# Kernel tuning notes

Hardware: AMD Instinct MI355X
Metric: run time of the kernel (lower is better)

The kernel has to match this reference:

```python
import jax, jax.numpy as jnp
import numpy as np

B, S, D, V = 512, 4096, 128, 6
SPARSITY = 0.1
PAD_IDX = 5


def setup_inputs() -> dict:
    key = jax.random.key(0)
    ks = jax.random.split(key, 16)
    n = lambda k, shape: (jax.random.normal(k, shape, jnp.float32) * 0.02)
    emb = n(ks[0], (V, D)).at[PAD_IDX].set(0.0)  # padding_idx=5 row zeroed
    # importance_network: D -> D/2 -> D/4 -> 1
    W1 = n(ks[1], (D, D // 2)); b1 = jnp.zeros((D // 2,), jnp.float32)
    W2 = n(ks[2], (D // 2, D // 4)); b2 = jnp.zeros((D // 4,), jnp.float32)
    W3 = n(ks[3], (D // 4, 1)); b3 = jnp.zeros((1,), jnp.float32)
    # attention_approximator: D -> D/2 -> D (dropout = identity in eval)
    A1 = n(ks[4], (D, D // 2)); a1 = jnp.zeros((D // 2,), jnp.float32)
    A2 = n(ks[5], (D // 2, D)); a2 = jnp.zeros((D,), jnp.float32)
    # classifier: D -> D/2 -> 1 -> sigmoid
    C1 = n(ks[6], (D, D // 2)); c1 = jnp.zeros((D // 2,), jnp.float32)
    C2 = n(ks[7], (D // 2, 1)); c2 = jnp.zeros((1,), jnp.float32)
    x = jax.random.randint(ks[8], (B, S), 0, V, dtype=jnp.int64 if jax.config.jax_enable_x64 else jnp.int32)
    return dict(x=x, emb=emb, W1=W1, b1=b1, W2=W2, b2=b2, W3=W3, b3=b3,
                A1=A1, a1=a1, A2=A2, a2=a2, C1=C1, c1=c1, C2=C2, c2=c2)


def reference(x, emb, W1, b1, W2, b2, W3, b3, A1, a1, A2, a2, C1, c1, C2, c2):
    batch, seq = x.shape
    k = max(1, int(seq * SPARSITY))  # 409
    e = emb[x]  # [B,S,D] embedding lookup
    # importance MLP + sigmoid -> learned scores [B,S]
    h = jax.nn.relu(e @ W1 + b1)
    h = jax.nn.relu(h @ W2 + b2)
    final_scores = jax.nn.sigmoid((h @ W3 + b3)[..., 0])  # [B,S]
    # topk select + gather embeddings (irregular access)
    top_vals, top_idx = jax.lax.top_k(final_scores, k)  # [B,k]
    sel = jnp.take_along_axis(e, top_idx[..., None], axis=1)  # [B,k,D]
    # attention approximator MLP
    attended = jax.nn.relu(sel @ A1 + a1) @ A2 + a2  # [B,k,D]
    pooled = attended.mean(axis=1)  # [B,D]
    # classifier
    pred = jax.nn.sigmoid((jax.nn.relu(pooled @ C1 + c1) @ C2 + c2))[..., 0]  # [B]
    return pred, top_idx, final_scores
```

## Files before the change

### kernel.cpp

```cpp
#include <hip/hip_runtime.h>
#include <hip/hip_bf16.h>
#include <math.h>

#define BB 512
#define SS 4096
#define DD 128
#define VV 6
#define KK 409



__global__ __launch_bounds__(256) void precompute_kernel(
    const float* __restrict__ emb,
    const float* __restrict__ W1, const float* __restrict__ b1,
    const float* __restrict__ W2, const float* __restrict__ b2,
    const float* __restrict__ W3, const float* __restrict__ b3,
    const float* __restrict__ A1, const float* __restrict__ a1,
    const float* __restrict__ A2, const float* __restrict__ a2,
    float* __restrict__ ws)
{
    __shared__ float sW1[DD * 64];
    __shared__ float sA1[DD * 64];
    __shared__ float sW2[64 * 32];
    __shared__ float sA2[64 * DD];
    __shared__ float sE[VV * DD];
    __shared__ float sW3[32];
    __shared__ float sb1[64], sb2[32], sa1[64], sa2[DD];
    __shared__ float sh1[VV * 64], sg[VV * 64], sh2[VV * 32];
    __shared__ float sb3;

    const int tid = threadIdx.x;

    {
        const float* srcs[9] = { W1, A1, W2, A2, emb, b1, b2, a1, a2 };
        float*       dsts[9] = { sW1, sA1, sW2, sA2, sE, sb1, sb2, sa1, sa2 };
        const int    ns[9]   = { 8192, 8192, 2048, 8192, VV*DD, 64, 32, 64, DD };
        for (int a = 0; a < 9; ++a) {
            const float4* s4 = (const float4*)srcs[a];
            float4* d4 = (float4*)dsts[a];
            const int n4 = ns[a] >> 2;
            for (int i = tid; i < n4; i += 256) d4[i] = s4[i];
        }
        if (tid < 32) sW3[tid] = W3[tid];
        if (tid == 0) sb3 = b3[0];
    }
    __syncthreads();

    for (int u = tid; u < 768; u += 256) {
        const int isH = (u < 384) ? 1 : 0;
        const int v = isH ? u : (u - 384);
        const int t = v >> 6, o = v & 63;
        const float* wcol = isH ? sW1 : sA1;
        float acc = isH ? sb1[o] : sa1[o];
        const float* ev = &sE[t * DD];
        #pragma unroll 8
        for (int d = 0; d < DD; ++d) acc += ev[d] * wcol[d * 64 + o];
        acc = fmaxf(acc, 0.f);
        if (isH) sh1[v] = acc; else sg[v] = acc;
    }
    __syncthreads();

    for (int u = tid; u < VV * 32; u += 256) {
        const int t = u >> 5, o = u & 31;
        float acc = sb2[o];
        #pragma unroll 8
        for (int j = 0; j < 64; ++j) acc += sh1[t * 64 + j] * sW2[j * 32 + o];
        sh2[u] = fmaxf(acc, 0.f);
    }
    __syncthreads();

    for (int u = tid; u < 6 + VV * DD; u += 256) {
        if (u < 6) {
            float s = sb3;
            #pragma unroll
            for (int j = 0; j < 32; ++j) s += sh2[u * 32 + j] * sW3[j];
            ws[u] = 1.f / (1.f + expf(-s));
        } else {
            const int v = u - 6;
            const int t = v >> 7, o = v & 127;
            float acc = sa2[o];
            #pragma unroll 8
            for (int j = 0; j < 64; ++j) acc += sg[t * 64 + j] * sA2[j * DD + o];
            ws[16 + v] = acc;
        }
    }
}

__global__ __launch_bounds__(512) void row_kernel(
    const int* __restrict__ x,
    const float* __restrict__ ws,
    const float* __restrict__ C1, const float* __restrict__ c1,
    const float* __restrict__ C2, const float* __restrict__ c2,
    float* __restrict__ pred, float* __restrict__ topk, float* __restrict__ fsc)
{
    __shared__ float sc[VV];
    __shared__ float att_s[VV * DD];
    __shared__ int   waveTot[8 * VV];
    __shared__ float pooled[DD];
    __shared__ float hcls[64];

    const int tid  = threadIdx.x;
    const int b    = blockIdx.x;
    const int lane = tid & 63;
    const int w    = tid >> 6;

    const int base = b * SS + tid * 8;
    const int4* xp = (const int4*)(x + base);
    int4 xv0 = xp[0], xv1 = xp[1];

    if (tid < VV) sc[tid] = ws[tid];
    for (int i = tid; i < VV * DD; i += 512) att_s[i] = ws[16 + i];
    __syncthreads();

    int vals[8];
    vals[0]=xv0.x; vals[1]=xv0.y; vals[2]=xv0.z; vals[3]=xv0.w;
    vals[4]=xv1.x; vals[5]=xv1.y; vals[6]=xv1.z; vals[7]=xv1.w;

    {
        float4* op = (float4*)(fsc + base);
        float4 o0, o1;
        o0.x = sc[vals[0]]; o0.y = sc[vals[1]]; o0.z = sc[vals[2]]; o0.w = sc[vals[3]];
        o1.x = sc[vals[4]]; o1.y = sc[vals[5]]; o1.z = sc[vals[6]]; o1.w = sc[vals[7]];
        op[0] = o0; op[1] = o1;
    }

    int lc[VV];
    #pragma unroll
    for (int t = 0; t < VV; ++t) {
        int c = 0;
        #pragma unroll
        for (int i = 0; i < 8; ++i) c += (vals[i] == t) ? 1 : 0;
        lc[t] = c;
    }

    int excl[VV];
    #pragma unroll
    for (int t = 0; t < VV; ++t) {
        int v = lc[t];
        #pragma unroll
        for (int off = 1; off < 64; off <<= 1) {
            int u = __shfl_up(v, off, 64);
            if (lane >= off) v += u;
        }
        excl[t] = v - lc[t];
        if (lane == 63) waveTot[w * VV + t] = v;
    }
    __syncthreads();

    int rowTot[VV], woff[VV];
    #pragma unroll
    for (int t = 0; t < VV; ++t) {
        int tot = 0, wo = 0;
        #pragma unroll
        for (int j = 0; j < 8; ++j) {
            int c = waveTot[j * VV + t];
            tot += c;
            if (j < 1) {}
            wo += (j < w) ? c : 0;
        }
        rowTot[t] = tot;
        woff[t] = wo;
    }

    float s_reg[VV];
    #pragma unroll
    for (int t = 0; t < VV; ++t) s_reg[t] = sc[t];
    int pri[VV];
    #pragma unroll
    for (int t = 0; t < VV; ++t) {
        int p = 0;
        #pragma unroll
        for (int u = 0; u < VV; ++u)
            p += ((s_reg[u] > s_reg[t]) || ((s_reg[u] == s_reg[t]) && (u < t))) ? 1 : 0;
        pri[t] = p;
    }
    int start[VV], m[VV];
    #pragma unroll
    for (int t = 0; t < VV; ++t) {
        int cb = 0;
        #pragma unroll
        for (int u = 0; u < VV; ++u)
            cb += (pri[u] < pri[t]) ? rowTot[u] : 0;
        int mm = KK - cb;
        mm = (mm < 0) ? 0 : mm;
        mm = (mm > rowTot[t]) ? rowTot[t] : mm;
        m[t] = mm;
        start[t] = cb + woff[t] + excl[t];
    }

    #pragma unroll
    for (int t = 0; t < VV; ++t) {
        int pos = start[t];
        #pragma unroll
        for (int i = 0; i < 8; ++i) {
            if (vals[i] == t) {
                if (pos < KK) topk[b * KK + pos] = (float)(tid * 8 + i);
                pos++;
            }
        }
    }

    if (tid < DD) {
        float acc = 0.f;
        #pragma unroll
        for (int t = 0; t < VV; ++t) acc += (float)m[t] * att_s[t * DD + tid];
        pooled[tid] = acc * (1.0f / (float)KK);
    }
    __syncthreads();
    if (tid < 64) {
        float acc = c1[tid];
        #pragma unroll 8
        for (int d = 0; d < DD; ++d) acc += pooled[d] * C1[d * 64 + tid];
        hcls[tid] = fmaxf(acc, 0.f);
    }
    __syncthreads();
    if (tid == 0) {
        float s = c2[0];
        #pragma unroll 8
        for (int j = 0; j < 64; ++j) s += hcls[j] * C2[j];
        pred[b] = 1.f / (1.f + expf(-s));
    }
}

extern "C" void kernel_launch(void* const* d_in, const int* in_sizes, int n_in,
                              void* d_out, int out_size, void* d_ws, size_t ws_size,
                              hipStream_t stream)
{
    (void)in_sizes; (void)n_in; (void)out_size; (void)ws_size;
    const int*   x   = (const int*)d_in[0];
    const float* emb = (const float*)d_in[1];
    const float* W1  = (const float*)d_in[2];
    const float* b1  = (const float*)d_in[3];
    const float* W2  = (const float*)d_in[4];
    const float* b2  = (const float*)d_in[5];
    const float* W3  = (const float*)d_in[6];
    const float* b3  = (const float*)d_in[7];
    const float* A1  = (const float*)d_in[8];
    const float* a1  = (const float*)d_in[9];
    const float* A2  = (const float*)d_in[10];
    const float* a2  = (const float*)d_in[11];
    const float* C1  = (const float*)d_in[12];
    const float* c1  = (const float*)d_in[13];
    const float* C2  = (const float*)d_in[14];
    const float* c2  = (const float*)d_in[15];

    float* out  = (float*)d_out;
    float* pred = out;
    float* topk = out + BB;
    float* fsc  = out + BB + BB*KK;
    float* ws   = (float*)d_ws;

    precompute_kernel<<<1, 256, 0, stream>>>(emb, W1, b1, W2, b2, W3, b3,
                                             A1, a1, A2, a2, ws);
    row_kernel<<<BB, 512, 0, stream>>>(x, ws, C1, c1, C2, c2, pred, topk, fsc);
}
```

Measured before the change: 113.1 us.

## Fuse precompute into row kernel and use ballot/mbcnt for per-token prefix counts

Merges the single-block precompute kernel into the per-row kernel, so each block recomputes the six-token MLP tables itself, reading the weights straight from global memory (served by L2). This removes a second launch and the serialized single-block dependency that the row kernel had to wait on. The shuffle-based inclusive scans are replaced with ballot plus mbcnt counting. The cost is redundant weight reads and MLP arithmetic in every one of the 512 blocks.

```diff
diff --git a/kernel.cpp b/kernel.cpp
--- a/kernel.cpp
+++ b/kernel.cpp
@@ -1,5 +1,4 @@
 #include <hip/hip_runtime.h>
-#include <hip/hip_bf16.h>
 #include <math.h>
 
 #define BB 512
@@ -9,48 +8,51 @@
 #define KK 409
 
 
-
-__global__ __launch_bounds__(256) void precompute_kernel(
+__global__ __launch_bounds__(512, 4) void fused_kernel(
+    const int* __restrict__ x,
     const float* __restrict__ emb,
     const float* __restrict__ W1, const float* __restrict__ b1,
     const float* __restrict__ W2, const float* __restrict__ b2,
     const float* __restrict__ W3, const float* __restrict__ b3,
     const float* __restrict__ A1, const float* __restrict__ a1,
     const float* __restrict__ A2, const float* __restrict__ a2,
-    float* __restrict__ ws)
+    const float* __restrict__ C1, const float* __restrict__ c1,
+    const float* __restrict__ C2, const float* __restrict__ c2,
+    float* __restrict__ pred, float* __restrict__ topk, float* __restrict__ fsc)
 {
-    __shared__ float sW1[DD * 64];
-    __shared__ float sA1[DD * 64];
-    __shared__ float sW2[64 * 32];
-    __shared__ float sA2[64 * DD];
     __shared__ float sE[VV * DD];
-    __shared__ float sW3[32];
-    __shared__ float sb1[64], sb2[32], sa1[64], sa2[DD];
+    __shared__ float sb1[64], sb2[32], sa1[64], sa2[DD], sW3[32];
     __shared__ float sh1[VV * 64], sg[VV * 64], sh2[VV * 32];
+    __shared__ float sc[VV];
+    __shared__ float att_s[VV * DD];
+    __shared__ int   waveTot[8 * 8];
+    __shared__ float pooled[DD];
+    __shared__ float hcls[64];
     __shared__ float sb3;
 
-    const int tid = threadIdx.x;
-
-    {
-        const float* srcs[9] = { W1, A1, W2, A2, emb, b1, b2, a1, a2 };
-        float*       dsts[9] = { sW1, sA1, sW2, sA2, sE, sb1, sb2, sa1, sa2 };
-        const int    ns[9]   = { 8192, 8192, 2048, 8192, VV*DD, 64, 32, 64, DD };
-        for (int a = 0; a < 9; ++a) {
-            const float4* s4 = (const float4*)srcs[a];
-            float4* d4 = (float4*)dsts[a];
-            const int n4 = ns[a] >> 2;
-            for (int i = tid; i < n4; i += 256) d4[i] = s4[i];
-        }
-        if (tid < 32) sW3[tid] = W3[tid];
-        if (tid == 0) sb3 = b3[0];
-    }
-    __syncthreads();
-
-    for (int u = tid; u < 768; u += 256) {
-        const int isH = (u < 384) ? 1 : 0;
-        const int v = isH ? u : (u - 384);
+    const int tid  = threadIdx.x;
+    const int b    = blockIdx.x;
+    const int lane = tid & 63;
+    const int w    = tid >> 6;
+
+    const int base = b * SS + tid * 8;
+    const int4* xp = (const int4*)(x + base);
+    int4 xv0 = xp[0], xv1 = xp[1];
+
+    for (int i = tid; i < VV * DD; i += 512) sE[i] = emb[i];
+    if (tid < 64)        sb1[tid]       = b1[tid];
+    else if (tid < 96)   sb2[tid - 64]  = b2[tid - 64];
+    else if (tid < 160)  sa1[tid - 96]  = a1[tid - 96];
+    else if (tid < 288)  sa2[tid - 160] = a2[tid - 160];
+    else if (tid < 320)  sW3[tid - 288] = W3[tid - 288];
+    else if (tid == 320) sb3 = b3[0];
+    __syncthreads();
+
+    for (int u = tid; u < 2 * VV * 64; u += 512) {
+        const int isH = (u < VV * 64) ? 1 : 0;
+        const int v = isH ? u : (u - VV * 64);
         const int t = v >> 6, o = v & 63;
-        const float* wcol = isH ? sW1 : sA1;
+        const float* wcol = isH ? W1 : A1;
         float acc = isH ? sb1[o] : sa1[o];
         const float* ev = &sE[t * DD];
         #pragma unroll 8
@@ -58,63 +60,66 @@
         acc = fmaxf(acc, 0.f);
         if (isH) sh1[v] = acc; else sg[v] = acc;
     }
-    __syncthreads();
-
-    for (int u = tid; u < VV * 32; u += 256) {
-        const int t = u >> 5, o = u & 31;
-        float acc = sb2[o];
-        #pragma unroll 8
-        for (int j = 0; j < 64; ++j) acc += sh1[t * 64 + j] * sW2[j * 32 + o];
-        sh2[u] = fmaxf(acc, 0.f);
-    }
-    __syncthreads();
-
-    for (int u = tid; u < 6 + VV * DD; u += 256) {
-        if (u < 6) {
-            float s = sb3;
-            #pragma unroll
-            for (int j = 0; j < 32; ++j) s += sh2[u * 32 + j] * sW3[j];
-            ws[u] = 1.f / (1.f + expf(-s));
+
+    int vals[8];
+    vals[0] = xv0.x; vals[1] = xv0.y; vals[2] = xv0.z; vals[3] = xv0.w;
+    vals[4] = xv1.x; vals[5] = xv1.y; vals[6] = xv1.z; vals[7] = xv1.w;
+
+    int excl[VV];
+    #pragma unroll
+    for (int t = 0; t < VV; ++t) {
+        int ex = 0, tot = 0;
+        #pragma unroll
+        for (int i = 0; i < 8; ++i) {
+            unsigned long long mk = __ballot(vals[i] == t);
+            ex += (int)__builtin_amdgcn_mbcnt_hi((unsigned)(mk >> 32),
+                       __builtin_amdgcn_mbcnt_lo((unsigned)mk, 0u));
+            tot += __popcll(mk);
+        }
+        excl[t] = ex;
+        if (lane == 0) waveTot[w * 8 + t] = tot;
+    }
+    __syncthreads();
+
+    for (int u = tid; u < VV * 32 + VV * DD; u += 512) {
+        if (u < VV * 32) {
+            const int t = u >> 5, o = u & 31;
+            float acc = sb2[o];
+            #pragma unroll 8
+            for (int j = 0; j < 64; ++j) acc += sh1[t * 64 + j] * W2[j * 32 + o];
+            sh2[u] = fmaxf(acc, 0.f);
         } else {
-            const int v = u - 6;
+            const int v = u - VV * 32;
             const int t = v >> 7, o = v & 127;
             float acc = sa2[o];
             #pragma unroll 8
-            for (int j = 0; j < 64; ++j) acc += sg[t * 64 + j] * sA2[j * DD + o];
-            ws[16 + v] = acc;
-        }
-    }
-}
-
-__global__ __launch_bounds__(512) void row_kernel(
-    const int* __restrict__ x,
-    const float* __restrict__ ws,
-    const float* __restrict__ C1, const float* __restrict__ c1,
-    const float* __restrict__ C2, const float* __restrict__ c2,
-    float* __restrict__ pred, float* __restrict__ topk, float* __restrict__ fsc)
-{
-    __shared__ float sc[VV];
-    __shared__ float att_s[VV * DD];
-    __shared__ int   waveTot[8 * VV];
-    __shared__ float pooled[DD];
-    __shared__ float hcls[64];
-
-    const int tid  = threadIdx.x;
-    const int b    = blockIdx.x;
-    const int lane = tid & 63;
-    const int w    = tid >> 6;
-
-    const int base = b * SS + tid * 8;
-    const int4* xp = (const int4*)(x + base);
-    int4 xv0 = xp[0], xv1 = xp[1];
-
-    if (tid < VV) sc[tid] = ws[tid];
-    for (int i = tid; i < VV * DD; i += 512) att_s[i] = ws[16 + i];
-    __syncthreads();
-
-    int vals[8];
-    vals[0]=xv0.x; vals[1]=xv0.y; vals[2]=xv0.z; vals[3]=xv0.w;
-    vals[4]=xv1.x; vals[5]=xv1.y; vals[6]=xv1.z; vals[7]=xv1.w;
+            for (int j = 0; j < 64; ++j) acc += sg[t * 64 + j] * A2[j * DD + o];
+            att_s[v] = acc;
+        }
+    }
+
+    int rowTot[VV], woff[VV];
+    #pragma unroll
+    for (int t = 0; t < VV; ++t) {
+        int tot = 0, wo = 0;
+        #pragma unroll
+        for (int j = 0; j < 8; ++j) {
+            int c = waveTot[j * 8 + t];
+            tot += c;
+            wo += (j < w) ? c : 0;
+        }
+        rowTot[t] = tot;
+        woff[t] = wo;
+    }
+    __syncthreads();
+
+    if (tid < VV) {
+        float s = sb3;
+        #pragma unroll
+        for (int j = 0; j < 32; ++j) s += sh2[tid * 32 + j] * sW3[j];
+        sc[tid] = 1.f / (1.f + expf(-s));
+    }
+    __syncthreads();
 
     {
         float4* op = (float4*)(fsc + base);
@@ -122,44 +127,6 @@
         o0.x = sc[vals[0]]; o0.y = sc[vals[1]]; o0.z = sc[vals[2]]; o0.w = sc[vals[3]];
         o1.x = sc[vals[4]]; o1.y = sc[vals[5]]; o1.z = sc[vals[6]]; o1.w = sc[vals[7]];
         op[0] = o0; op[1] = o1;
-    }
-
-    int lc[VV];
-    #pragma unroll
-    for (int t = 0; t < VV; ++t) {
-        int c = 0;
-        #pragma unroll
-        for (int i = 0; i < 8; ++i) c += (vals[i] == t) ? 1 : 0;
-        lc[t] = c;
-    }
-
-    int excl[VV];
-    #pragma unroll
-    for (int t = 0; t < VV; ++t) {
-        int v = lc[t];
-        #pragma unroll
-        for (int off = 1; off < 64; off <<= 1) {
-            int u = __shfl_up(v, off, 64);
-            if (lane >= off) v += u;
-        }
-        excl[t] = v - lc[t];
-        if (lane == 63) waveTot[w * VV + t] = v;
-    }
-    __syncthreads();
-
-    int rowTot[VV], woff[VV];
-    #pragma unroll
-    for (int t = 0; t < VV; ++t) {
-        int tot = 0, wo = 0;
-        #pragma unroll
-        for (int j = 0; j < 8; ++j) {
-            int c = waveTot[j * VV + t];
-            tot += c;
-            if (j < 1) {}
-            wo += (j < w) ? c : 0;
-        }
-        rowTot[t] = tot;
-        woff[t] = wo;
     }
 
     float s_reg[VV];
@@ -188,14 +155,17 @@
         start[t] = cb + woff[t] + excl[t];
     }
 
-    #pragma unroll
-    for (int t = 0; t < VV; ++t) {
-        int pos = start[t];
-        #pragma unroll
-        for (int i = 0; i < 8; ++i) {
-            if (vals[i] == t) {
-                if (pos < KK) topk[b * KK + pos] = (float)(tid * 8 + i);
-                pos++;
+    {
+        float* trow = topk + b * KK;
+        #pragma unroll
+        for (int t = 0; t < VV; ++t) {
+            int pos = start[t];
+            #pragma unroll
+            for (int i = 0; i < 8; ++i) {
+                if (vals[i] == t) {
+                    if (pos < KK) trow[pos] = (float)(tid * 8 + i);
+                    pos++;
+                }
             }
         }
     }
@@ -226,7 +196,7 @@
                               void* d_out, int out_size, void* d_ws, size_t ws_size,
                               hipStream_t stream)
 {
-    (void)in_sizes; (void)n_in; (void)out_size; (void)ws_size;
+    (void)in_sizes; (void)n_in; (void)out_size; (void)d_ws; (void)ws_size;
     const int*   x   = (const int*)d_in[0];
     const float* emb = (const float*)d_in[1];
     const float* W1  = (const float*)d_in[2];
@@ -248,9 +218,8 @@
     float* pred = out;
     float* topk = out + BB;
     float* fsc  = out + BB + BB*KK;
-    float* ws   = (float*)d_ws;
-
-    precompute_kernel<<<1, 256, 0, stream>>>(emb, W1, b1, W2, b2, W3, b3,
-                                             A1, a1, A2, a2, ws);
-    row_kernel<<<BB, 512, 0, stream>>>(x, ws, C1, c1, C2, c2, pred, topk, fsc);
+
+    fused_kernel<<<BB, 512, 0, stream>>>(x, emb, W1, b1, W2, b2, W3, b3,
+                                         A1, a1, A2, a2, C1, c1, C2, c2,
+                                         pred, topk, fsc);
 }
```

New measurement: 111.4 us. About the same (-1.5%).
